# Kernel tuning notes

Measured on AMD Instinct MI355X. Metric: run time of the kernel, lower is better.

Reference implementation:

```python
import jax, jax.numpy as jnp
import numpy as np

EPS = 1e-16  # torch.clamp(squared_distance, min=1e-16)


def knn_interpolate(x, pos_x, pos_y, k):
    """Faithful jax version of Mesh_Reduced.knn_interpolate.

    x:     [Nx, C]  features at source nodes
    pos_x: [Nx, 3]  source positions
    pos_y: [Ny, 3]  query positions
    Returns [Ny, C].
    """
    # Brute-force knn (replaces torch_cluster.knn). Use the expanded form
    # ||y||^2 + ||x||^2 - 2 y.x to avoid a [Ny, Nx, 3] intermediate.
    d2 = (
        jnp.sum(pos_y * pos_y, axis=-1)[:, None]
        + jnp.sum(pos_x * pos_x, axis=-1)[None, :]
        - 2.0 * pos_y @ pos_x.T
    )  # [Ny, Nx]
    _, x_idx = jax.lax.top_k(-d2, k)  # [Ny, k] nearest source indices per query

    # Exact squared distance on the selected neighbors (matches torch numerics:
    # diff = pos_x[x_idx] - pos_y[y_idx]).
    diff = pos_x[x_idx] - pos_y[:, None, :]           # [Ny, k, 3]
    sq = jnp.sum(diff * diff, axis=-1, keepdims=True)  # [Ny, k, 1]
    w = 1.0 / jnp.clip(sq, EPS)                        # inverse-distance weights

    xg = x[x_idx]                                      # gather: [Ny, k, C]
    # scatter-sum over the k neighbors of each query == reduce over axis 1
    num = jnp.sum(xg * w, axis=1)                      # [Ny, C]
    den = jnp.sum(w, axis=1)                           # [Ny, 1]
    return (num / den).astype(jnp.float32)


def setup_inputs() -> dict:
    key = jax.random.key(0)
    k1, k2, k3 = jax.random.split(key, 3)
    N_PIVOTAL, N_MESH, C = 2048, 65536, 16
    return {
        "x": jax.random.normal(k1, (N_PIVOTAL, C), dtype=jnp.float32),
        "pos_x": jax.random.uniform(k2, (N_PIVOTAL, 3), dtype=jnp.float32),
        "pos_y": jax.random.uniform(k3, (N_MESH, 3), dtype=jnp.float32),
        "k": 3,
    }


def reference(x, pos_x, pos_y, k):
    return knn_interpolate(x, pos_x, pos_y, k)
```

## Files before the change

### kernel.cpp

```cpp
#include <hip/hip_runtime.h>
#include <stdint.h>

#define NXP   2048
#define NC    16
#define GD    8
#define NCELL (GD*GD*GD)
#define BBLK  512
#define QBLK  512
#define SEG   8
#define QPB   (QBLK / SEG)
#define QGRID 512

#define WS_SPT   0
#define WS_SIDX  32768
#define WS_CST   40960

__device__ __forceinline__ int cell_of(float v) {
    int c = (int)(v * (float)GD);
    c = c > GD - 1 ? GD - 1 : c;
    return c < 0 ? 0 : c;
}

__device__ __forceinline__ uint32_t mono(float d) {
    uint32_t b = __float_as_uint(d);
    return b ^ (uint32_t)(((int32_t)b >> 31) | 0x80000000);
}
__device__ __forceinline__ float unmono(uint32_t m) {
    uint32_t b = (m & 0x80000000u) ? (m ^ 0x80000000u) : ~m;
    return __uint_as_float(b);
}

__device__ __forceinline__ void ins_fast(uint64_t k, uint64_t& b0, uint64_t& b1, uint64_t& b2) {
    const bool lt0 = k < b0, lt1 = k < b1;
    b2 = lt1 ? b1 : k;
    b1 = lt0 ? b0 : (lt1 ? k : b1);
    b0 = lt0 ? k  : b0;
}

__device__ __forceinline__ void ins_dedup(uint64_t k, uint64_t& b0, uint64_t& b1, uint64_t& b2) {
    if (k == b0 || k == b1 || k == b2) return;
    const bool lt0 = k < b0, lt1 = k < b1, lt2 = k < b2;
    b2 = lt1 ? b1 : (lt2 ? k : b2);
    b1 = lt0 ? b0 : (lt1 ? k : b1);
    b0 = lt0 ? k  : b0;
}

__device__ __forceinline__ uint64_t shfl_xor_u64(uint64_t v, int mask) {
    const int lo = __shfl_xor((int)(uint32_t)v, mask);
    const int hi = __shfl_xor((int)(uint32_t)(v >> 32), mask);
    return ((uint64_t)(uint32_t)hi << 32) | (uint32_t)lo;
}

__device__ __forceinline__ void merge_group(uint64_t& b0, uint64_t& b1, uint64_t& b2) {
    #pragma unroll
    for (int mask = 1; mask < SEG; mask <<= 1) {
        const uint64_t r0 = shfl_xor_u64(b0, mask);
        const uint64_t r1 = shfl_xor_u64(b1, mask);
        const uint64_t r2 = shfl_xor_u64(b2, mask);
        ins_dedup(r0, b0, b1, b2);
        ins_dedup(r1, b0, b1, b2);
        ins_dedup(r2, b0, b1, b2);
    }
}

__global__ __launch_bounds__(BBLK) void build_grid(
    const float* __restrict__ pos_x,
    float4* __restrict__ wspt, int* __restrict__ wsidx, int* __restrict__ wcstart)
{
    __shared__ int sA[NCELL];
    __shared__ int cur[NCELL];
    const int t = threadIdx.x;

    sA[t] = 0;
    __syncthreads();

    const float4* px4 = (const float4*)pos_x;
    const float4 v0 = px4[t*3+0], v1 = px4[t*3+1], v2 = px4[t*3+2];
    const float pxx[4] = {v0.x, v0.w, v1.z, v2.y};
    const float pyy[4] = {v0.y, v1.x, v1.w, v2.z};
    const float pzz[4] = {v0.z, v1.y, v2.x, v2.w};
    int cc[4];
    #pragma unroll
    for (int i = 0; i < 4; ++i) {
        cc[i] = (cell_of(pzz[i]) * GD + cell_of(pyy[i])) * GD + cell_of(pxx[i]);
        atomicAdd(&sA[cc[i]], 1);
    }
    __syncthreads();

    if (t < 64) {
        const int base = t * 8;
        int v[8];
        int run = 0;
        #pragma unroll
        for (int i = 0; i < 8; ++i) { run += sA[base + i]; v[i] = run; }
        int xs = run;
        #pragma unroll
        for (int off = 1; off < 64; off <<= 1) {
            const int y = __shfl_up(xs, off);
            if (t >= off) xs += y;
        }
        const int excl = xs - run;
        #pragma unroll
        for (int i = 0; i < 8; ++i) {
            const int inc = excl + v[i];
            wcstart[base + i + 1] = inc;
            cur[base + i] = inc - sA[base + i];
        }
        if (t == 0) wcstart[0] = 0;
    }
    __syncthreads();

    #pragma unroll
    for (int i = 0; i < 4; ++i) {
        const int p = t * 4 + i;
        const int pos = atomicAdd(&cur[cc[i]], 1);
        const float sx = __fadd_rn(__fadd_rn(__fmul_rn(pxx[i], pxx[i]),
                                             __fmul_rn(pyy[i], pyy[i])),
                                   __fmul_rn(pzz[i], pzz[i]));
        wspt[pos] = make_float4(pxx[i], pyy[i], pzz[i], sx);
        wsidx[pos] = p;
    }
}

__global__ __launch_bounds__(QBLK) void knn_query(
    const float* __restrict__ x,
    const float* __restrict__ pos_x,
    const float* __restrict__ pos_y,
    const float4* __restrict__ wspt, const int* __restrict__ wsidx,
    const int* __restrict__ wcstart,
    float* __restrict__ out,
    int ny)
{
    __shared__ float4 spt[NXP];
    __shared__ int    sidx[NXP];
    __shared__ int    cstart[NCELL + 1];

    const int t = threadIdx.x;

    #pragma unroll
    for (int i = t; i < NXP; i += QBLK) spt[i] = wspt[i];
    #pragma unroll
    for (int i = t; i < NXP; i += QBLK) sidx[i] = wsidx[i];
    for (int i = t; i < NCELL + 1; i += QBLK) cstart[i] = wcstart[i];
    __syncthreads();

    const int s = t & (SEG - 1);
    const int nbatch = (ny + QPB - 1) / QPB;

    for (int batch = blockIdx.x; batch < nbatch; batch += gridDim.x) {
        const int q = batch * QPB + (t >> 3);
        if (q >= ny) continue;

        const float y0 = pos_y[q*3+0], y1 = pos_y[q*3+1], y2 = pos_y[q*3+2];
        const float sy = __fadd_rn(__fadd_rn(__fmul_rn(y0, y0), __fmul_rn(y1, y1)),
                                   __fmul_rn(y2, y2));
        const int cx = cell_of(y0), cy = cell_of(y1), cz = cell_of(y2);

        uint64_t b0 = ~0ull, b1 = ~0ull, b2 = ~0ull;

#define EVAL_BODY(P, INS)                                                       \
        {                                                                       \
            const float4 pt = spt[P];                                           \
            const float dot = __fmaf_rn(y2, pt.z,                               \
                              __fmaf_rn(y1, pt.y, __fmul_rn(y0, pt.x)));        \
            const float d = __fmaf_rn(-2.0f, dot, __fadd_rn(sy, pt.w));         \
            const uint64_t kk = ((uint64_t)mono(d) << 32) | (uint32_t)sidx[P];  \
            if (kk < b2) INS(kk, b0, b1, b2);                                   \
        }

        const int x0 = cx - 1 < 0 ? 0 : cx - 1;
        const int x1 = cx + 1 > GD - 1 ? GD - 1 : cx + 1;
        #pragma unroll
        for (int r = 0; r < 9; ++r) {
            const int uz = cz + r / 3 - 1, uy = cy + r % 3 - 1;
            int st = 0, en = 0;
            if (((unsigned)uz < (unsigned)GD) & ((unsigned)uy < (unsigned)GD)) {
                const int cb = (uz * GD + uy) * GD;
                st = cstart[cb + x0];
                en = cstart[cb + x1 + 1];
            }
            for (int p = st + s; p < en; p += SEG) EVAL_BODY(p, ins_fast)
        }
        merge_group(b0, b1, b2);

        {
            bool have3 = (b2 != ~0ull);
            float b2d = unmono((uint32_t)(b2 >> 32));
            if (!(have3 && (b2d + 1e-4f < 0.015625f))) {
                for (int r = 0; r < 25; ++r) {
                    const int dzi = r / 5 - 2, dyi = r % 5 - 2;
                    const int uz = cz + dzi, uy = cy + dyi;
                    if (((unsigned)uz >= (unsigned)GD) | ((unsigned)uy >= (unsigned)GD))
                        continue;
                    const int cb = (uz * GD + uy) * GD;
                    if (dzi == -2 || dzi == 2 || dyi == -2 || dyi == 2) {
                        const int xa = cx - 2 < 0 ? 0 : cx - 2;
                        const int xb = cx + 2 > GD - 1 ? GD - 1 : cx + 2;
                        const int st = cstart[cb + xa], en = cstart[cb + xb + 1];
                        for (int p = st + s; p < en; p += SEG) EVAL_BODY(p, ins_fast)
                    } else {
                        if (cx - 2 >= 0) {
                            const int st = cstart[cb + cx - 2], en = cstart[cb + cx - 1];
                            for (int p = st + s; p < en; p += SEG) EVAL_BODY(p, ins_fast)
                        }
                        if (cx + 2 <= GD - 1) {
                            const int st = cstart[cb + cx + 2], en = cstart[cb + cx + 3];
                            for (int p = st + s; p < en; p += SEG) EVAL_BODY(p, ins_fast)
                        }
                    }
                }
                merge_group(b0, b1, b2);

                have3 = (b2 != ~0ull);
                b2d = unmono((uint32_t)(b2 >> 32));
                if (!(have3 && (b2d + 1e-4f < 0.0625f))) {
                    for (int p = s; p < NXP; p += SEG) EVAL_BODY(p, ins_dedup)
                    merge_group(b0, b1, b2);
                }
            }
        }
#undef EVAL_BODY

        const int j[3] = { (int)(uint32_t)b0, (int)(uint32_t)b1, (int)(uint32_t)b2 };
        float w[3];
        #pragma unroll
        for (int i = 0; i < 3; ++i) {
            const int jj = j[i];
            const float ax = pos_x[jj*3+0], ay = pos_x[jj*3+1], az = pos_x[jj*3+2];
            const float dx = __fsub_rn(ax, y0);
            const float dy = __fsub_rn(ay, y1);
            const float dz = __fsub_rn(az, y2);
            const float sq = __fadd_rn(__fadd_rn(__fmul_rn(dx, dx), __fmul_rn(dy, dy)),
                                       __fmul_rn(dz, dz));
            w[i] = 1.0f / fmaxf(sq, 1e-16f);
        }
        const float inv_den = 1.0f / __fadd_rn(__fadd_rn(w[0], w[1]), w[2]);

        const float2* x2 = (const float2*)x;
        float2* o2 = (float2*)out;
        const float2 a = x2[j[0]*8 + s];
        const float2 b = x2[j[1]*8 + s];
        const float2 c = x2[j[2]*8 + s];
        float2 rr;
        rr.x = (w[0]*a.x + w[1]*b.x + w[2]*c.x) * inv_den;
        rr.y = (w[0]*a.y + w[1]*b.y + w[2]*c.y) * inv_den;
        o2[q*8 + s] = rr;
    }
}

extern "C" void kernel_launch(void* const* d_in, const int* in_sizes, int n_in,
                              void* d_out, int out_size, void* d_ws, size_t ws_size,
                              hipStream_t stream) {
    const float* x     = (const float*)d_in[0];
    const float* pos_x = (const float*)d_in[1];
    const float* pos_y = (const float*)d_in[2];

    float* out = (float*)d_out;
    const int ny = in_sizes[2] / 3;

    float4* wspt   = (float4*)((char*)d_ws + WS_SPT);
    int*    wsidx  = (int*)   ((char*)d_ws + WS_SIDX);
    int*    wcst   = (int*)   ((char*)d_ws + WS_CST);

    build_grid<<<1, BBLK, 0, stream>>>(pos_x, wspt, wsidx, wcst);

    knn_query<<<QGRID, QBLK, 0, stream>>>(x, pos_x, pos_y, wspt, wsidx, wcst, out, ny);
}
```

Baseline: 33.93 us.

## Bin queries by grid cell and process each cell's queries per block

Adds a counting sort of query points into grid cells (histogram, scan, scatter) and a new per-cell kernel. The kernel loads only the candidate neighbourhood for its cell into shared memory and evaluates it with one query per thread, so the per-segment shuffle merges go away. An exact clearance test per query decides whether a wave-cooperative full scan is needed, and the old kernel stays as a fallback when the workspace is too small. This trades three extra small launches and a scatter pass for better locality and less redundant candidate loading per block, and boundary cells with a larger radius may cause load imbalance.

New measurement: 61.09 us. 1.8x slower.

```diff
diff --git a/kernel.cpp b/kernel.cpp
--- a/kernel.cpp
+++ b/kernel.cpp
@@ -6,14 +6,16 @@
 #define GD    8
 #define NCELL (GD*GD*GD)
 #define BBLK  512
-#define QBLK  512
-#define SEG   8
-#define QPB   (QBLK / SEG)
-#define QGRID 512
-
-#define WS_SPT   0
-#define WS_SIDX  32768
-#define WS_CST   40960
+#define CAP   512
+#define HCELL 0.125f
+
+#define WS_SPT    0
+#define WS_SIDX   32768
+#define WS_CST    40960
+#define WS_QBIN   44032
+#define WS_QSTART 46080
+#define WS_QCUR   48640
+#define WS_QIDX   50688
 
 __device__ __forceinline__ int cell_of(float v) {
     int c = (int)(v * (float)GD);
@@ -36,7 +38,6 @@
     b1 = lt0 ? b0 : (lt1 ? k : b1);
     b0 = lt0 ? k  : b0;
 }
-
 __device__ __forceinline__ void ins_dedup(uint64_t k, uint64_t& b0, uint64_t& b1, uint64_t& b2) {
     if (k == b0 || k == b1 || k == b2) return;
     const bool lt0 = k < b0, lt1 = k < b1, lt2 = k < b2;
@@ -44,34 +45,28 @@
     b1 = lt0 ? b0 : (lt1 ? k : b1);
     b0 = lt0 ? k  : b0;
 }
-
+__device__ __forceinline__ uint64_t shfl_u64(uint64_t v, int src) {
+    const int lo = __shfl((int)(uint32_t)v, src);
+    const int hi = __shfl((int)(uint32_t)(v >> 32), src);
+    return ((uint64_t)(uint32_t)hi << 32) | (uint32_t)lo;
+}
 __device__ __forceinline__ uint64_t shfl_xor_u64(uint64_t v, int mask) {
     const int lo = __shfl_xor((int)(uint32_t)v, mask);
     const int hi = __shfl_xor((int)(uint32_t)(v >> 32), mask);
     return ((uint64_t)(uint32_t)hi << 32) | (uint32_t)lo;
 }
 
-__device__ __forceinline__ void merge_group(uint64_t& b0, uint64_t& b1, uint64_t& b2) {
-    #pragma unroll
-    for (int mask = 1; mask < SEG; mask <<= 1) {
-        const uint64_t r0 = shfl_xor_u64(b0, mask);
-        const uint64_t r1 = shfl_xor_u64(b1, mask);
-        const uint64_t r2 = shfl_xor_u64(b2, mask);
-        ins_dedup(r0, b0, b1, b2);
-        ins_dedup(r1, b0, b1, b2);
-        ins_dedup(r2, b0, b1, b2);
-    }
-}
-
 __global__ __launch_bounds__(BBLK) void build_grid(
     const float* __restrict__ pos_x,
-    float4* __restrict__ wspt, int* __restrict__ wsidx, int* __restrict__ wcstart)
+    float4* __restrict__ wspt, int* __restrict__ wsidx, int* __restrict__ wcstart,
+    int* __restrict__ qbins, int zeroq)
 {
     __shared__ int sA[NCELL];
     __shared__ int cur[NCELL];
     const int t = threadIdx.x;
 
     sA[t] = 0;
+    if (zeroq) qbins[t] = 0;
     __syncthreads();
 
     const float4* px4 = (const float4*)pos_x;
@@ -122,24 +117,262 @@
     }
 }
 
-__global__ __launch_bounds__(QBLK) void knn_query(
+__global__ __launch_bounds__(256) void qhist(
+    const float* __restrict__ pos_y, int ny, int* __restrict__ qbins)
+{
+    __shared__ int h[NCELL];
+    const int t = threadIdx.x;
+    h[t] = 0; h[t + 256] = 0;
+    __syncthreads();
+    for (int q = blockIdx.x * 256 + t; q < ny; q += gridDim.x * 256) {
+        const int c = (cell_of(pos_y[q*3+2]) * GD + cell_of(pos_y[q*3+1])) * GD
+                    + cell_of(pos_y[q*3+0]);
+        atomicAdd(&h[c], 1);
+    }
+    __syncthreads();
+    if (h[t])       atomicAdd(&qbins[t], h[t]);
+    if (h[t + 256]) atomicAdd(&qbins[t + 256], h[t + 256]);
+}
+
+__global__ __launch_bounds__(64) void qscan(
+    const int* __restrict__ qbins, int* __restrict__ qstart, int* __restrict__ qcur)
+{
+    const int t = threadIdx.x;
+    const int base = t * 8;
+    int v[8];
+    int run = 0;
+    #pragma unroll
+    for (int i = 0; i < 8; ++i) { run += qbins[base + i]; v[i] = run; }
+    int xs = run;
+    #pragma unroll
+    for (int off = 1; off < 64; off <<= 1) {
+        const int y = __shfl_up(xs, off);
+        if (t >= off) xs += y;
+    }
+    const int excl = xs - run;
+    #pragma unroll
+    for (int i = 0; i < 8; ++i) {
+        const int inc = excl + v[i];
+        qstart[base + i + 1] = inc;
+        qcur[base + i] = inc - qbins[base + i];
+    }
+    if (t == 0) qstart[0] = 0;
+}
+
+__global__ __launch_bounds__(256) void qscatter(
+    const float* __restrict__ pos_y, int ny,
+    int* __restrict__ qcur, int* __restrict__ qidx)
+{
+    for (int q = blockIdx.x * 256 + threadIdx.x; q < ny; q += gridDim.x * 256) {
+        const int c = (cell_of(pos_y[q*3+2]) * GD + cell_of(pos_y[q*3+1])) * GD
+                    + cell_of(pos_y[q*3+0]);
+        qidx[atomicAdd(&qcur[c], 1)] = q;
+    }
+}
+
+__global__ __launch_bounds__(256) void knn_cell(
     const float* __restrict__ x,
     const float* __restrict__ pos_x,
     const float* __restrict__ pos_y,
     const float4* __restrict__ wspt, const int* __restrict__ wsidx,
+    const int* __restrict__ wcst,
+    const int* __restrict__ qstart, const int* __restrict__ qidx,
+    float* __restrict__ out)
+{
+    __shared__ float4 scand[CAP];
+    __shared__ int    scidx[CAP];
+    __shared__ int    rst[25], roff[26];
+    __shared__ int    sL, sLpad, sForce;
+
+    const int t = threadIdx.x;
+    const int c = blockIdx.x >> 1, half = blockIdx.x & 1;
+    const int cx = c & 7, cy = (c >> 3) & 7, cz = c >> 6;
+
+    const int bcnt = (int)(cx == 0 || cx == GD-1) + (int)(cy == 0 || cy == GD-1)
+                   + (int)(cz == 0 || cz == GD-1);
+    const int R  = (bcnt >= 2) ? 2 : 1;
+    const int W  = 2 * R + 1;
+    const int NR = W * W;
+
+    if (t < NR) {
+        const int uz = cz + t / W - R, uy = cy + t % W - R;
+        int st = 0, len = 0;
+        if (((unsigned)uz < (unsigned)GD) & ((unsigned)uy < (unsigned)GD)) {
+            const int xa = cx - R < 0 ? 0 : cx - R;
+            const int xb = cx + R > GD - 1 ? GD - 1 : cx + R;
+            const int cb = (uz * GD + uy) * GD;
+            st  = wcst[cb + xa];
+            len = wcst[cb + xb + 1] - st;
+        }
+        rst[t] = st;
+        roff[t] = len;
+    }
+    __syncthreads();
+    if (t == 0) {
+        int o = 0;
+        #pragma unroll 1
+        for (int r = 0; r < NR; ++r) { const int l = roff[r]; roff[r] = o; o += l; }
+        roff[NR] = o;
+        const int lt = o > CAP ? CAP : o;
+        sL = lt;
+        sLpad = (lt + 3) & ~3;
+        sForce = (o > CAP) ? 1 : 0;
+    }
+    __syncthreads();
+
+    const int L = sL, Lpad = sLpad, force = sForce;
+    for (int i = t; i < L; i += 256) {
+        int r = 0;
+        while (i >= roff[r + 1]) ++r;
+        const int src = rst[r] + (i - roff[r]);
+        scand[i] = wspt[src];
+        scidx[i] = wsidx[src];
+    }
+    for (int i = L + t; i < Lpad; i += 256) {
+        scand[i] = make_float4(0.f, 0.f, 0.f, 3e30f);
+        scidx[i] = 0x7fffffff;
+    }
+    __syncthreads();
+
+    const int wave = t >> 6, lane = t & 63;
+    const int qs = qstart[c], qe = qstart[c + 1];
+    const int mid = qs + ((qe - qs + 1) >> 1);
+    const int beg = half ? mid : qs;
+    const int end = half ? qe  : mid;
+
+    for (int i0 = beg + wave * 64; i0 < end; i0 += 4 * 64) {
+        const int slot = i0 + lane;
+        const bool active = slot < end;
+        const int q = active ? qidx[slot] : 0;
+        float y0 = 0.f, y1 = 0.f, y2 = 0.f;
+        if (active) { y0 = pos_y[q*3+0]; y1 = pos_y[q*3+1]; y2 = pos_y[q*3+2]; }
+        const float sy = __fadd_rn(__fadd_rn(__fmul_rn(y0, y0), __fmul_rn(y1, y1)),
+                                   __fmul_rn(y2, y2));
+
+        float clr = 1e30f;
+        if (cx - R > 0)      clr = fminf(clr, y0 - (float)(cx - R) * HCELL);
+        if (cx + R < GD - 1) clr = fminf(clr, (float)(cx + R + 1) * HCELL - y0);
+        if (cy - R > 0)      clr = fminf(clr, y1 - (float)(cy - R) * HCELL);
+        if (cy + R < GD - 1) clr = fminf(clr, (float)(cy + R + 1) * HCELL - y1);
+        if (cz - R > 0)      clr = fminf(clr, y2 - (float)(cz - R) * HCELL);
+        if (cz + R < GD - 1) clr = fminf(clr, (float)(cz + R + 1) * HCELL - y2);
+        const float thr = clr * clr;
+
+        uint64_t b0 = ~0ull, b1 = ~0ull, b2 = ~0ull;
+
+        for (int j = 0; j < Lpad; j += 4) {
+            #pragma unroll
+            for (int u = 0; u < 4; ++u) {
+                const float4 pt = scand[j + u];
+                const int oi = scidx[j + u];
+                const float dot = __fmaf_rn(y2, pt.z,
+                                  __fmaf_rn(y1, pt.y, __fmul_rn(y0, pt.x)));
+                const float d = __fmaf_rn(-2.0f, dot, __fadd_rn(sy, pt.w));
+                const uint64_t kk = ((uint64_t)mono(d) << 32) | (uint32_t)oi;
+                const bool lt0 = kk < b0, lt1 = kk < b1, lt2 = kk < b2;
+                b2 = lt1 ? b1 : (lt2 ? kk : b2);
+                b1 = lt0 ? b0 : (lt1 ? kk : b1);
+                b0 = lt0 ? kk : b0;
+            }
+        }
+
+        bool esc = false;
+        if (active) {
+            const bool have3 = (b2 != ~0ull);
+            const float b2d = unmono((uint32_t)(b2 >> 32));
+            esc = !(have3 && (b2d + 1e-4f < thr)) | (force != 0);
+        }
+        unsigned long long bal = __ballot(esc);
+        while (bal) {
+            const int e = __ffsll(bal) - 1;
+            bal &= bal - 1;
+            const float ey0 = __shfl(y0, e), ey1 = __shfl(y1, e), ey2 = __shfl(y2, e);
+            const float esy = __shfl(sy, e);
+            uint64_t m0 = shfl_u64(b0, e), m1 = shfl_u64(b1, e), m2 = shfl_u64(b2, e);
+            for (int p = lane; p < NXP; p += 64) {
+                const float4 pt = wspt[p];
+                const float dot = __fmaf_rn(ey2, pt.z,
+                                  __fmaf_rn(ey1, pt.y, __fmul_rn(ey0, pt.x)));
+                const float d = __fmaf_rn(-2.0f, dot, __fadd_rn(esy, pt.w));
+                const uint64_t kk = ((uint64_t)mono(d) << 32) | (uint32_t)wsidx[p];
+                if (kk < m2) ins_dedup(kk, m0, m1, m2);
+            }
+            #pragma unroll
+            for (int mask = 1; mask < 64; mask <<= 1) {
+                const uint64_t r0 = shfl_xor_u64(m0, mask);
+                const uint64_t r1 = shfl_xor_u64(m1, mask);
+                const uint64_t r2 = shfl_xor_u64(m2, mask);
+                ins_dedup(r0, m0, m1, m2);
+                ins_dedup(r1, m0, m1, m2);
+                ins_dedup(r2, m0, m1, m2);
+            }
+            if (lane == e) { b0 = m0; b1 = m1; b2 = m2; }
+        }
+
+        if (active) {
+            const int j[3] = { (int)(uint32_t)b0, (int)(uint32_t)b1, (int)(uint32_t)b2 };
+            float w[3];
+            #pragma unroll
+            for (int i = 0; i < 3; ++i) {
+                const int jj = j[i];
+                const float ax = pos_x[jj*3+0], ay = pos_x[jj*3+1], az = pos_x[jj*3+2];
+                const float dx = __fsub_rn(ax, y0);
+                const float dy = __fsub_rn(ay, y1);
+                const float dz = __fsub_rn(az, y2);
+                const float sq = __fadd_rn(__fadd_rn(__fmul_rn(dx, dx), __fmul_rn(dy, dy)),
+                                           __fmul_rn(dz, dz));
+                w[i] = 1.0f / fmaxf(sq, 1e-16f);
+            }
+            const float inv_den = 1.0f / __fadd_rn(__fadd_rn(w[0], w[1]), w[2]);
+
+            const float4* x4 = (const float4*)x;
+            float4* o4 = (float4*)out;
+            #pragma unroll
+            for (int tt = 0; tt < 4; ++tt) {
+                const float4 a = x4[j[0]*4 + tt];
+                const float4 b = x4[j[1]*4 + tt];
+                const float4 cc = x4[j[2]*4 + tt];
+                float4 r;
+                r.x = (w[0]*a.x + w[1]*b.x + w[2]*cc.x) * inv_den;
+                r.y = (w[0]*a.y + w[1]*b.y + w[2]*cc.y) * inv_den;
+                r.z = (w[0]*a.z + w[1]*b.z + w[2]*cc.z) * inv_den;
+                r.w = (w[0]*a.w + w[1]*b.w + w[2]*cc.w) * inv_den;
+                o4[q*4 + tt] = r;
+            }
+        }
+    }
+}
+
+#define QBLK  512
+#define SEG   8
+#define QPB   (QBLK / SEG)
+#define QGRID 512
+
+__device__ __forceinline__ void merge_group8(uint64_t& b0, uint64_t& b1, uint64_t& b2) {
+    #pragma unroll
+    for (int mask = 1; mask < SEG; mask <<= 1) {
+        const uint64_t r0 = shfl_xor_u64(b0, mask);
+        const uint64_t r1 = shfl_xor_u64(b1, mask);
+        const uint64_t r2 = shfl_xor_u64(b2, mask);
+        ins_dedup(r0, b0, b1, b2);
+        ins_dedup(r1, b0, b1, b2);
+        ins_dedup(r2, b0, b1, b2);
+    }
+}
+
+__global__ __launch_bounds__(QBLK) void knn_query_fb(
+    const float* __restrict__ x, const float* __restrict__ pos_x,
+    const float* __restrict__ pos_y,
+    const float4* __restrict__ wspt, const int* __restrict__ wsidx,
     const int* __restrict__ wcstart,
-    float* __restrict__ out,
-    int ny)
+    float* __restrict__ out, int ny)
 {
     __shared__ float4 spt[NXP];
     __shared__ int    sidx[NXP];
     __shared__ int    cstart[NCELL + 1];
 
     const int t = threadIdx.x;
-
-    #pragma unroll
     for (int i = t; i < NXP; i += QBLK) spt[i] = wspt[i];
-    #pragma unroll
     for (int i = t; i < NXP; i += QBLK) sidx[i] = wsidx[i];
     for (int i = t; i < NCELL + 1; i += QBLK) cstart[i] = wcstart[i];
     __syncthreads();
@@ -181,7 +414,7 @@
             }
             for (int p = st + s; p < en; p += SEG) EVAL_BODY(p, ins_fast)
         }
-        merge_group(b0, b1, b2);
+        merge_group8(b0, b1, b2);
 
         {
             bool have3 = (b2 != ~0ull);
@@ -209,13 +442,13 @@
                         }
                     }
                 }
-                merge_group(b0, b1, b2);
+                merge_group8(b0, b1, b2);
 
                 have3 = (b2 != ~0ull);
                 b2d = unmono((uint32_t)(b2 >> 32));
                 if (!(have3 && (b2d + 1e-4f < 0.0625f))) {
                     for (int p = s; p < NXP; p += SEG) EVAL_BODY(p, ins_dedup)
-                    merge_group(b0, b1, b2);
+                    merge_group8(b0, b1, b2);
                 }
             }
         }
@@ -254,15 +487,30 @@
     const float* x     = (const float*)d_in[0];
     const float* pos_x = (const float*)d_in[1];
     const float* pos_y = (const float*)d_in[2];
-
     float* out = (float*)d_out;
     const int ny = in_sizes[2] / 3;
 
     float4* wspt   = (float4*)((char*)d_ws + WS_SPT);
     int*    wsidx  = (int*)   ((char*)d_ws + WS_SIDX);
     int*    wcst   = (int*)   ((char*)d_ws + WS_CST);
-
-    build_grid<<<1, BBLK, 0, stream>>>(pos_x, wspt, wsidx, wcst);
-
-    knn_query<<<QGRID, QBLK, 0, stream>>>(x, pos_x, pos_y, wspt, wsidx, wcst, out, ny);
-}
+    int*    qbins  = (int*)   ((char*)d_ws + WS_QBIN);
+    int*    qstart = (int*)   ((char*)d_ws + WS_QSTART);
+    int*    qcur   = (int*)   ((char*)d_ws + WS_QCUR);
+    int*    qidx   = (int*)   ((char*)d_ws + WS_QIDX);
+
+    const size_t need = (size_t)WS_QIDX + (size_t)ny * 4;
+
+    if (ws_size >= need) {
+        build_grid<<<1, BBLK, 0, stream>>>(pos_x, wspt, wsidx, wcst, qbins, 1);
+        const int hblocks = (ny + 255) / 256;
+        qhist<<<hblocks, 256, 0, stream>>>(pos_y, ny, qbins);
+        qscan<<<1, 64, 0, stream>>>(qbins, qstart, qcur);
+        qscatter<<<hblocks, 256, 0, stream>>>(pos_y, ny, qcur, qidx);
+        knn_cell<<<NCELL * 2, 256, 0, stream>>>(x, pos_x, pos_y, wspt, wsidx, wcst,
+                                                qstart, qidx, out);
+    } else {
+        build_grid<<<1, BBLK, 0, stream>>>(pos_x, wspt, wsidx, wcst, qbins, 0);
+        knn_query_fb<<<QGRID, QBLK, 0, stream>>>(x, pos_x, pos_y, wspt, wsidx, wcst,
+                                                 out, ny);
+    }
+}
```
